# Performance work log

Hardware: AMD Instinct MI355X
Metric: run time of the kernel (lower is better)

The kernel has to match this reference:

```python
import jax, jax.numpy as jnp
import numpy as np

N = 50000          # num nodes
E = 800000         # num edges (before self loops)
F = 128            # input feature dim
UNITS = 128        # output units
ATT_UNITS = 128    # attention units (Q/K dim)
HEADS = 8


def setup_inputs() -> dict:
    key = jax.random.key(0)
    ks = jax.random.split(key, 6)
    s = 1.0 / np.sqrt(F).astype(np.float32)  # ~glorot scale
    return {
        "x": jax.random.normal(ks[0], (N, F), dtype=jnp.float32),
        "edge_index": jax.random.randint(ks[1], (2, E), 0, N, dtype=jnp.int32),
        "query_kernel": jax.random.normal(ks[2], (F, ATT_UNITS), dtype=jnp.float32) * s,
        "query_bias": jnp.zeros((ATT_UNITS,), jnp.float32),
        "key_kernel": jax.random.normal(ks[3], (F, ATT_UNITS), dtype=jnp.float32) * s,
        "key_bias": jnp.zeros((ATT_UNITS,), jnp.float32),
        "kernel": jax.random.normal(ks[4], (F, UNITS), dtype=jnp.float32) * s,
        "bias": jnp.zeros((UNITS,), jnp.float32),
    }


def segment_softmax(scores, seg, num_segments):
    # scores: [E', H], seg: [E'] -> softmax over edges sharing the same target node, per head
    smax = jax.ops.segment_max(scores, seg, num_segments=num_segments)
    sexp = jnp.exp(scores - smax[seg])
    ssum = jax.ops.segment_sum(sexp, seg, num_segments=num_segments)
    return sexp / ssum[seg]


def reference(x, edge_index, query_kernel, query_bias, key_kernel, key_bias, kernel, bias):
    num_nodes = x.shape[0]
    # add self-loop edges (as in tf_geometric add_self_loop_edge)
    loop = jnp.arange(num_nodes, dtype=edge_index.dtype)
    row = jnp.concatenate([edge_index[0], loop])  # target nodes, [E']
    col = jnp.concatenate([edge_index[1], loop])  # source nodes, [E']

    Q = jax.nn.relu(x @ query_kernel + query_bias)[row]  # [E', A]
    K = jax.nn.relu(x @ key_kernel + key_bias)[col]      # [E', A]
    V = (x @ kernel)[col]                                 # [E', U]

    # split into attention heads: tf.split(..., num_heads, axis=-1)
    Qh = Q.reshape(-1, HEADS, ATT_UNITS // HEADS)
    Kh = K.reshape(-1, HEADS, ATT_UNITS // HEADS)
    att = jnp.sum(Qh * Kh, axis=-1)                       # [E', H]
    alpha = segment_softmax(att, row, num_nodes)          # [E', H]

    # split_value_heads=True: split V into head slices, weight, scatter-add, concat
    Vh = V.reshape(-1, HEADS, UNITS // HEADS)             # [E', H, U/H]
    msg = Vh * alpha[:, :, None]
    out = jax.ops.segment_sum(msg, row, num_segments=num_nodes)  # [N, H, U/H]
    out = out.reshape(num_nodes, UNITS)
    out = out + bias  # use_bias=True, activation=None
    return out
```

## Files before the change

### kernel.cpp

```cpp
#include <hip/hip_runtime.h>
#include <hip/hip_fp16.h>
#include <cstdint>

#define FDIM 128
#define XSTR 136
#define NROWTILE 128
#define WCHUNKS ((FDIM * XSTR * 2) / 1024)
#define CSRS 128

typedef __attribute__((ext_vector_type(8))) _Float16 half8;
typedef __attribute__((ext_vector_type(2))) _Float16 h2;
typedef __attribute__((ext_vector_type(16))) float float16;

#if defined(__has_builtin)
#if __has_builtin(__builtin_amdgcn_fdot2)
#define HAVE_FDOT2 1
#endif
#endif

__device__ __forceinline__ void gload_lds16(const void* g, void* s) {
    __builtin_amdgcn_global_load_lds(
        (const __attribute__((address_space(1))) void*)g,
        (__attribute__((address_space(3))) void*)s, 16, 0, 0);
}

__device__ __forceinline__ h2 as_h2(unsigned u) {
    union { unsigned u; h2 h; } c; c.u = u; return c.h;
}
__device__ __forceinline__ float2 h2_to_f2(unsigned u) {
    __half2 h = *(__half2*)&u;
    return __half22float2(h);
}

__global__ __launch_bounds__(256) void edges_k(
    const int* __restrict__ ei, int E,
    const float* __restrict__ Wq, const float* __restrict__ Wk,
    const float* __restrict__ Wv, __half* __restrict__ WTH,
    int* __restrict__ deg, int* __restrict__ csr)
{
    int idx = blockIdx.x * 256 + threadIdx.x;

    if (idx < 3 * FDIM * FDIM) {
        int mat = idx >> 14;
        int m = idx & 16383;
        int k = m >> 7;
        int nn = m & 127;
        const float* __restrict__ W = (mat == 0) ? Wq : (mat == 1) ? Wk : Wv;
        WTH[(size_t)mat * FDIM * XSTR + nn * XSTR + k] =
            __float2half_rn(W[k * FDIM + nn]);
    }

    if (idx < E) {
        int row = ei[idx];
        int col = ei[E + idx];
        int slot = atomicAdd(&deg[row], 1);
        if (slot < CSRS) csr[(row << 7) + slot] = col;
    }
}

__global__ __launch_bounds__(256) void gemm_mfma_k(
    const float* __restrict__ x, const __half* __restrict__ WTH,
    const float* __restrict__ bq, const float* __restrict__ bk,
    const float* __restrict__ bias,
    __half* __restrict__ Qb, uint2* __restrict__ KV, int N)
{
    __shared__ __half xs[NROWTILE * XSTR];
    __shared__ __half ws[FDIM * XSTR];

    const int tid  = threadIdx.x;
    const int wave = tid >> 6;
    const int lane = tid & 63;
    const int r0   = blockIdx.x * NROWTILE;

    for (int c = wave; c < WCHUNKS; c += 4)
        gload_lds16((const char*)WTH + c * 1024 + lane * 16, (char*)ws + c * 1024);

    #pragma unroll
    for (int it = 0; it < 16; ++it) {
        int idx = it * 256 + tid;
        int row = idx >> 5;
        int c4 = (idx & 31) << 2;
        float4 v = make_float4(0.f, 0.f, 0.f, 0.f);
        if (r0 + row < N) v = *(const float4*)(x + (size_t)(r0 + row) * FDIM + c4);
        __half h[4] = {__float2half_rn(v.x), __float2half_rn(v.y),
                       __float2half_rn(v.z), __float2half_rn(v.w)};
        *(ushort4*)(xs + row * XSTR + c4) = *(ushort4*)h;
    }

    const int mrow = lane & 31;
    const int half = lane >> 5;
    const int arow = wave * 32 + mrow;

    for (int mat = 0; mat < 3; ++mat) {
        __syncthreads();

        float16 acc[4];
        #pragma unroll
        for (int nt = 0; nt < 4; ++nt)
            #pragma unroll
            for (int r = 0; r < 16; ++r) acc[nt][r] = 0.f;

        #pragma unroll
        for (int ks = 0; ks < 8; ++ks) {
            const int ko = ks * 16 + half * 8;
            half8 ah = *(const half8*)(xs + arow * XSTR + ko);
            #pragma unroll
            for (int nt = 0; nt < 4; ++nt) {
                half8 bh = *(const half8*)(ws + (nt * 32 + mrow) * XSTR + ko);
                acc[nt] = __builtin_amdgcn_mfma_f32_32x32x16_f16(ah, bh, acc[nt], 0, 0, 0);
            }
        }

        __syncthreads();

        const float* bvec = (mat == 0) ? bq : (mat == 1) ? bk : bias;
        #pragma unroll
        for (int nt = 0; nt < 4; ++nt) {
            const int col = nt * 32 + mrow;
            const float bb = bvec[col];
            #pragma unroll
            for (int reg = 0; reg < 16; ++reg) {
                int rl = wave * 32 + (reg & 3) + 8 * (reg >> 2) + 4 * half;
                float v = acc[nt][reg] + bb;
                if (mat < 2) v = fmaxf(v, 0.f);
                ws[rl * XSTR + col] = __float2half_rn(v);
            }
        }
        __syncthreads();

        if (mat == 0) {
            #pragma unroll
            for (int it = 0; it < 8; ++it) {
                int idx = it * 256 + tid;
                int row = idx >> 4;
                int c = (idx & 15) * 8;
                uint4 v = *(const uint4*)(ws + row * XSTR + c);
                if (r0 + row < N)
                    *(uint4*)(Qb + (size_t)(r0 + row) * FDIM + c) = v;
            }
        } else {
            __half* kvh = (__half*)KV;
            const int sub = (mat == 2) ? 2 : 0;
            #pragma unroll
            for (int it = 0; it < 32; ++it) {
                int idx = it * 256 + tid;
                int row = idx >> 6;
                int p = idx & 63;
                unsigned v = *(const unsigned*)(ws + row * XSTR + 2 * p);
                if (r0 + row < N)
                    *(unsigned*)(kvh + (size_t)(r0 + row) * 256 + p * 4 + sub) = v;
            }
        }

        if (mat < 2) {
            __syncthreads();
            const char* nh = (const char*)(WTH + (size_t)(mat + 1) * FDIM * XSTR);
            for (int c = wave; c < WCHUNKS; c += 4)
                gload_lds16(nh + c * 1024 + lane * 16, (char*)ws + c * 1024);
        }
    }
}

__global__ __launch_bounds__(256) void aggregate_k(
    const __half* __restrict__ Qb, const uint2* __restrict__ KV,
    const int* __restrict__ deg, const int* __restrict__ csr,
    float* __restrict__ out, int N)
{
    const int lane = threadIdx.x & 63;
    int n = blockIdx.x * 4 + (threadIdx.x >> 6);
    if (n >= N) return;
    n = __builtin_amdgcn_readfirstlane(n);

    int d = __builtin_amdgcn_readfirstlane(deg[n]);
    if (d > CSRS) d = CSRS;
    const int off   = n << 7;
    const int total = d + 1;

    const unsigned qu = *(const unsigned*)(Qb + (size_t)n * FDIM + 2 * lane);
    const h2 q2 = as_h2(qu);
    const float2 qf = h2_to_f2(qu);
    (void)qf; (void)q2;

    float acc0 = 0.f, acc1 = 0.f, lsum = 0.f;

    auto proc = [&](uint2 kv) {
#ifdef HAVE_FDOT2
        float p = __builtin_amdgcn_fdot2(as_h2(kv.x), q2, 0.0f, false);
#else
        float2 kf = h2_to_f2(kv.x);
        float p = qf.x * kf.x + qf.y * kf.y;
#endif
        p += __shfl_xor(p, 1);
        p += __shfl_xor(p, 2);
        p += __shfl_xor(p, 4);
        float s = __expf(p);
        float2 vf = h2_to_f2(kv.y);
        lsum += s;
        acc0 += s * vf.x;
        acc1 += s * vf.y;
    };

    int idxbuf[8];
    #pragma unroll
    for (int u = 0; u < 8; ++u)
        idxbuf[u] = (u == 0) ? n : ((u < total) ? csr[off + u - 1] : 0);

    int t = 0;
    while (t + 8 <= total) {
        uint2 kv[8];
        #pragma unroll
        for (int u = 0; u < 8; ++u)
            kv[u] = KV[(((unsigned)idxbuf[u]) << 6) + lane];
        #pragma unroll
        for (int u = 0; u < 8; ++u) {
            int nx = t + 8 + u;
            idxbuf[u] = (nx < total) ? csr[off + nx - 1] : 0;
        }
        #pragma unroll
        for (int u = 0; u < 8; ++u) proc(kv[u]);
        t += 8;
    }
    for (; t < total; ++t) {
        int c = (t == 0) ? n : csr[off + t - 1];
        uint2 kv = KV[(((unsigned)c) << 6) + lane];
        proc(kv);
    }

    const float inv = 1.0f / lsum;
    float2 o;
    o.x = acc0 * inv;
    o.y = acc1 * inv;
    *(float2*)(out + (size_t)n * FDIM + 2 * lane) = o;
}

extern "C" void kernel_launch(void* const* d_in, const int* in_sizes, int n_in,
                              void* d_out, int out_size, void* d_ws, size_t ws_size,
                              hipStream_t stream)
{
    const float* x    = (const float*)d_in[0];
    const int*   ei   = (const int*)d_in[1];
    const float* Wq   = (const float*)d_in[2];
    const float* bq   = (const float*)d_in[3];
    const float* Wk   = (const float*)d_in[4];
    const float* bk   = (const float*)d_in[5];
    const float* Wv   = (const float*)d_in[6];
    const float* bias = (const float*)d_in[7];
    float* out = (float*)d_out;

    const int N = in_sizes[0] / FDIM;
    const int E = in_sizes[1] / 2;
    const int nblk = (N + NROWTILE - 1) / NROWTILE;

    __half* WTH = (__half*)d_ws;
    __half* Qb  = WTH + (size_t)3 * FDIM * XSTR;
    uint2*  KV  = (uint2*)(Qb + (size_t)N * FDIM);
    int* deg    = (int*)(KV + (size_t)N * 64);
    int* csr    = deg + N;

    (void)hipMemsetAsync(deg, 0, (size_t)N * sizeof(int), stream);

    int ework = (E > 3 * FDIM * FDIM) ? E : 3 * FDIM * FDIM;
    edges_k<<<(ework + 255) / 256, 256, 0, stream>>>(
        ei, E, Wq, Wk, Wv, WTH, deg, csr);

    gemm_mfma_k<<<nblk, 256, 0, stream>>>(x, WTH, bq, bk, bias, Qb, KV, N);

    aggregate_k<<<(N + 3) / 4, 256, 0, stream>>>(Qb, KV, deg, csr, out, N);
}
```

Baseline: 221.9 us.

## Pre-convert x to fp16 and split GEMM across three matrices via grid

The fp32-to-fp16 conversion of x moves into the edges kernel, which writes a padded, strided fp16 copy into workspace. The GEMM kernel now launches a 2D grid with one y-slice per weight matrix (Q, K, V) instead of looping over the three matrices inside each block. Each block loads its x tile and weight tile straight into LDS with async global-to-LDS copies. The aim is roughly three times as many GEMM blocks to fill the CUs, plus no register-side conversion inside the GEMM. The cost is extra global traffic: the fp16 x copy is written once and read three times, and the edges kernel grid grows to cover all padded rows.

```diff
diff --git a/kernel.cpp b/kernel.cpp
--- a/kernel.cpp
+++ b/kernel.cpp
@@ -6,6 +6,7 @@
 #define XSTR 136
 #define NROWTILE 128
 #define WCHUNKS ((FDIM * XSTR * 2) / 1024)
+#define XCHUNKS ((NROWTILE * XSTR * 2) / 1024)
 #define CSRS 128
 
 typedef __attribute__((ext_vector_type(8))) _Float16 half8;
@@ -33,12 +34,23 @@
 }
 
 __global__ __launch_bounds__(256) void edges_k(
+    const float* __restrict__ x, __half* __restrict__ XH,
     const int* __restrict__ ei, int E,
     const float* __restrict__ Wq, const float* __restrict__ Wk,
     const float* __restrict__ Wv, __half* __restrict__ WTH,
-    int* __restrict__ deg, int* __restrict__ csr)
+    int* __restrict__ deg, int* __restrict__ csr, int N, int Npad)
 {
     int idx = blockIdx.x * 256 + threadIdx.x;
+
+    if (idx < Npad * 32) {
+        int row = idx >> 5;
+        int c = (idx & 31) << 2;
+        float4 v = make_float4(0.f, 0.f, 0.f, 0.f);
+        if (row < N) v = *(const float4*)(x + (size_t)row * FDIM + c);
+        __half h[4] = {__float2half_rn(v.x), __float2half_rn(v.y),
+                       __float2half_rn(v.z), __float2half_rn(v.w)};
+        *(ushort4*)(XH + (size_t)row * XSTR + c) = *(ushort4*)h;
+    }
 
     if (idx < 3 * FDIM * FDIM) {
         int mat = idx >> 14;
@@ -59,7 +71,7 @@
 }
 
 __global__ __launch_bounds__(256) void gemm_mfma_k(
-    const float* __restrict__ x, const __half* __restrict__ WTH,
+    const __half* __restrict__ XH, const __half* __restrict__ WTH,
     const float* __restrict__ bq, const float* __restrict__ bk,
     const float* __restrict__ bias,
     __half* __restrict__ Qb, uint2* __restrict__ KV, int N)
@@ -71,92 +83,75 @@
     const int wave = tid >> 6;
     const int lane = tid & 63;
     const int r0   = blockIdx.x * NROWTILE;
-
-    for (int c = wave; c < WCHUNKS; c += 4)
-        gload_lds16((const char*)WTH + c * 1024 + lane * 16, (char*)ws + c * 1024);
-
-    #pragma unroll
-    for (int it = 0; it < 16; ++it) {
-        int idx = it * 256 + tid;
-        int row = idx >> 5;
-        int c4 = (idx & 31) << 2;
-        float4 v = make_float4(0.f, 0.f, 0.f, 0.f);
-        if (r0 + row < N) v = *(const float4*)(x + (size_t)(r0 + row) * FDIM + c4);
-        __half h[4] = {__float2half_rn(v.x), __float2half_rn(v.y),
-                       __float2half_rn(v.z), __float2half_rn(v.w)};
-        *(ushort4*)(xs + row * XSTR + c4) = *(ushort4*)h;
-    }
+    const int mat  = blockIdx.y;
+
+    const char* wbase = (const char*)(WTH + (size_t)mat * FDIM * XSTR);
+    for (int c = wave; c < XCHUNKS; c += 4) {
+        gload_lds16((const char*)(XH + (size_t)r0 * XSTR) + c * 1024 + lane * 16,
+                    (char*)xs + c * 1024);
+        gload_lds16(wbase + c * 1024 + lane * 16, (char*)ws + c * 1024);
+    }
+    __syncthreads();
 
     const int mrow = lane & 31;
     const int half = lane >> 5;
     const int arow = wave * 32 + mrow;
 
-    for (int mat = 0; mat < 3; ++mat) {
-        __syncthreads();
-
-        float16 acc[4];
-        #pragma unroll
-        for (int nt = 0; nt < 4; ++nt)
-            #pragma unroll
-            for (int r = 0; r < 16; ++r) acc[nt][r] = 0.f;
-
-        #pragma unroll
-        for (int ks = 0; ks < 8; ++ks) {
-            const int ko = ks * 16 + half * 8;
-            half8 ah = *(const half8*)(xs + arow * XSTR + ko);
-            #pragma unroll
-            for (int nt = 0; nt < 4; ++nt) {
-                half8 bh = *(const half8*)(ws + (nt * 32 + mrow) * XSTR + ko);
-                acc[nt] = __builtin_amdgcn_mfma_f32_32x32x16_f16(ah, bh, acc[nt], 0, 0, 0);
-            }
-        }
-
-        __syncthreads();
-
-        const float* bvec = (mat == 0) ? bq : (mat == 1) ? bk : bias;
+    float16 acc[4];
+    #pragma unroll
+    for (int nt = 0; nt < 4; ++nt)
+        #pragma unroll
+        for (int r = 0; r < 16; ++r) acc[nt][r] = 0.f;
+
+    #pragma unroll
+    for (int ks = 0; ks < 8; ++ks) {
+        const int ko = ks * 16 + half * 8;
+        half8 ah = *(const half8*)(xs + arow * XSTR + ko);
         #pragma unroll
         for (int nt = 0; nt < 4; ++nt) {
-            const int col = nt * 32 + mrow;
-            const float bb = bvec[col];
-            #pragma unroll
-            for (int reg = 0; reg < 16; ++reg) {
-                int rl = wave * 32 + (reg & 3) + 8 * (reg >> 2) + 4 * half;
-                float v = acc[nt][reg] + bb;
-                if (mat < 2) v = fmaxf(v, 0.f);
-                ws[rl * XSTR + col] = __float2half_rn(v);
-            }
-        }
-        __syncthreads();
-
-        if (mat == 0) {
-            #pragma unroll
-            for (int it = 0; it < 8; ++it) {
-                int idx = it * 256 + tid;
-                int row = idx >> 4;
-                int c = (idx & 15) * 8;
-                uint4 v = *(const uint4*)(ws + row * XSTR + c);
-                if (r0 + row < N)
-                    *(uint4*)(Qb + (size_t)(r0 + row) * FDIM + c) = v;
-            }
-        } else {
-            __half* kvh = (__half*)KV;
-            const int sub = (mat == 2) ? 2 : 0;
-            #pragma unroll
-            for (int it = 0; it < 32; ++it) {
-                int idx = it * 256 + tid;
-                int row = idx >> 6;
-                int p = idx & 63;
-                unsigned v = *(const unsigned*)(ws + row * XSTR + 2 * p);
-                if (r0 + row < N)
-                    *(unsigned*)(kvh + (size_t)(r0 + row) * 256 + p * 4 + sub) = v;
-            }
-        }
-
-        if (mat < 2) {
-            __syncthreads();
-            const char* nh = (const char*)(WTH + (size_t)(mat + 1) * FDIM * XSTR);
-            for (int c = wave; c < WCHUNKS; c += 4)
-                gload_lds16(nh + c * 1024 + lane * 16, (char*)ws + c * 1024);
+            half8 bh = *(const half8*)(ws + (nt * 32 + mrow) * XSTR + ko);
+            acc[nt] = __builtin_amdgcn_mfma_f32_32x32x16_f16(ah, bh, acc[nt], 0, 0, 0);
+        }
+    }
+
+    __syncthreads();
+
+    const float* bvec = (mat == 0) ? bq : (mat == 1) ? bk : bias;
+    #pragma unroll
+    for (int nt = 0; nt < 4; ++nt) {
+        const int col = nt * 32 + mrow;
+        const float bb = bvec[col];
+        #pragma unroll
+        for (int reg = 0; reg < 16; ++reg) {
+            int rl = wave * 32 + (reg & 3) + 8 * (reg >> 2) + 4 * half;
+            float v = acc[nt][reg] + bb;
+            if (mat < 2) v = fmaxf(v, 0.f);
+            ws[rl * XSTR + col] = __float2half_rn(v);
+        }
+    }
+    __syncthreads();
+
+    if (mat == 0) {
+        #pragma unroll
+        for (int it = 0; it < 8; ++it) {
+            int idx = it * 256 + tid;
+            int row = idx >> 4;
+            int c = (idx & 15) * 8;
+            uint4 v = *(const uint4*)(ws + row * XSTR + c);
+            if (r0 + row < N)
+                *(uint4*)(Qb + (size_t)(r0 + row) * FDIM + c) = v;
+        }
+    } else {
+        __half* kvh = (__half*)KV;
+        const int sub = (mat == 2) ? 2 : 0;
+        #pragma unroll
+        for (int it = 0; it < 32; ++it) {
+            int idx = it * 256 + tid;
+            int row = idx >> 6;
+            int p = idx & 63;
+            unsigned v = *(const unsigned*)(ws + row * XSTR + 2 * p);
+            if (r0 + row < N)
+                *(unsigned*)(kvh + (size_t)(r0 + row) * 256 + p * 4 + sub) = v;
         }
     }
 }
@@ -250,20 +245,22 @@
     const int N = in_sizes[0] / FDIM;
     const int E = in_sizes[1] / 2;
     const int nblk = (N + NROWTILE - 1) / NROWTILE;
+    const int Npad = nblk * NROWTILE;
 
     __half* WTH = (__half*)d_ws;
-    __half* Qb  = WTH + (size_t)3 * FDIM * XSTR;
+    __half* XH  = WTH + (size_t)3 * FDIM * XSTR;
+    __half* Qb  = XH + (size_t)Npad * XSTR;
     uint2*  KV  = (uint2*)(Qb + (size_t)N * FDIM);
     int* deg    = (int*)(KV + (size_t)N * 64);
     int* csr    = deg + N;
 
     (void)hipMemsetAsync(deg, 0, (size_t)N * sizeof(int), stream);
 
-    int ework = (E > 3 * FDIM * FDIM) ? E : 3 * FDIM * FDIM;
-    edges_k<<<(ework + 255) / 256, 256, 0, stream>>>(
-        ei, E, Wq, Wk, Wv, WTH, deg, csr);
-
-    gemm_mfma_k<<<nblk, 256, 0, stream>>>(x, WTH, bq, bk, bias, Qb, KV, N);
+    edges_k<<<(Npad * 32 + 255) / 256, 256, 0, stream>>>(
+        x, XH, ei, E, Wq, Wk, Wv, WTH, deg, csr, N, Npad);
+
+    gemm_mfma_k<<<dim3(nblk, 3), 256, 0, stream>>>(
+        XH, WTH, bq, bk, bias, Qb, KV, N);
 
     aggregate_k<<<(N + 3) / 4, 256, 0, stream>>>(Qb, KV, deg, csr, out, N);
 }
```

New measurement: 220.1 us. No clear change (-0.8%).
